# Kernel optimization log

Hardware: AMD Instinct MI355X
Metric: run time of the kernel (lower is better)

Reference implementation:

```python
import jax, jax.numpy as jnp
import numpy as np

N = 100000      # nodes
E = 1600000     # edges (avg degree 16)
IN_FEATS = 128
HEADS = 4
OUT_FEATS = 16
NEG_SLOPE = 0.2
EPS = 1e-16


def setup_inputs() -> dict:
    key = jax.random.key(0)
    k1, k2, k3, k4, k5, k6 = jax.random.split(key, 6)
    feat = jax.random.normal(k1, (N, IN_FEATS), dtype=jnp.float32)
    # xavier-ish scale for params
    W = jax.random.normal(k2, (IN_FEATS, HEADS * OUT_FEATS), dtype=jnp.float32) * 0.1
    attn_l = jax.random.normal(k3, (1, HEADS, OUT_FEATS), dtype=jnp.float32) * 0.1
    attn_r = jax.random.normal(k4, (1, HEADS, OUT_FEATS), dtype=jnp.float32) * 0.1
    src_index = jax.random.randint(k5, (E,), 0, N, dtype=jnp.int32)
    trg_index = jax.random.randint(k6, (E,), 0, N, dtype=jnp.int32)
    return {"feat": feat, "W": W, "attn_l": attn_l, "attn_r": attn_r,
            "src_index": src_index, "trg_index": trg_index}


def reference(feat, W, attn_l, attn_r, src_index, trg_index):
    # dropout layers are identity in eval mode
    n = feat.shape[0]
    h = (feat @ W).reshape(n, HEADS, OUT_FEATS)            # [N,H,F]
    el = jnp.sum(h * attn_l, axis=-1)                      # [N,H]
    er = jnp.sum(h * attn_r, axis=-1)                      # [N,H]
    s = el[src_index] + er[trg_index]                      # [E,H] edge scores
    s = jnp.where(s > 0, s, NEG_SLOPE * s)                 # LeakyReLU(0.2)
    # neighborhood-aware softmax over incoming edges of each target node
    s = s - jnp.max(s)                                     # global max shift (as in source)
    e = jnp.exp(s)                                         # [E,H]
    denom = jax.ops.segment_sum(e, trg_index, num_segments=n)  # [N,H]
    attn = e / (denom[trg_index] + EPS)                    # [E,H]
    # weighted aggregation of lifted source features into target nodes
    msg = h[src_index] * attn[:, :, None]                  # [E,H,F]
    h_prime = jax.ops.segment_sum(msg, trg_index, num_segments=n)  # [N,H,F]
    return h_prime.reshape(n, HEADS * OUT_FEATS)
```

## Files before the change

kernel.cpp:

```cpp
#include <hip/hip_runtime.h>

typedef unsigned short ushort_t;
typedef __attribute__((ext_vector_type(8))) short bf16x8;
typedef __attribute__((ext_vector_type(4))) float f32x4v;

#define EPB 8000

static __device__ __forceinline__ float bf2f(ushort_t u) {
  union { unsigned int i; float f; } v; v.i = ((unsigned int)u) << 16; return v.f;
}
static __device__ __forceinline__ ushort_t f2bf(float f) {
  union { float f; unsigned int i; } v; v.f = f;
  unsigned int r = v.i + 0x7FFFu + ((v.i >> 16) & 1u);
  return (ushort_t)(r >> 16);
}
static __device__ __forceinline__ float leaky(float s) {
  return s > 0.f ? s : 0.2f * s;
}

__global__ __launch_bounds__(256) void packw_hist(
    const float* __restrict__ W, const float* __restrict__ attnl,
    const float* __restrict__ attnr, ushort_t* __restrict__ wfrag,
    const int* __restrict__ trg, int E, int nbkt,
    int* __restrict__ blockHist, int nb3)
{
  const int b = blockIdx.x;
  const int t = threadIdx.x;
  if (b == nb3) {
    const int kc = t >> 6, l = t & 63;
    const int q = l >> 4, n = l & 15;
    #pragma unroll
    for (int tile = 0; tile < 5; ++tile) {
      #pragma unroll
      for (int j = 0; j < 8; ++j) {
        const int k = kc * 32 + q * 8 + j;
        float v = 0.f;
        if (tile < 4) {
          v = W[k * 64 + tile * 16 + n];
        } else if (n < 4) {
          for (int f = 0; f < 16; ++f)
            v += W[k * 64 + n * 16 + f] * attnl[n * 16 + f];
        } else if (n < 8) {
          const int hd = n - 4;
          for (int f = 0; f < 16; ++f)
            v += W[k * 64 + hd * 16 + f] * attnr[hd * 16 + f];
        }
        wfrag[((tile * 4 + kc) * 64 + l) * 8 + j] = f2bf(v);
      }
    }
    return;
  }
  __shared__ int hist[256];
  hist[t] = 0;
  __syncthreads();
  const int start = b * EPB;
  const int end = min(start + EPB, E);
  for (int e = start + t; e < end; e += 256)
    atomicAdd(&hist[trg[e] >> 9], 1);
  __syncthreads();
  if (t < nbkt) blockHist[b * nbkt + t] = hist[t];
}

__global__ __launch_bounds__(64) void bucket_scan(
    int* __restrict__ blockHist, int nb3, int nbkt, int* __restrict__ colTotal)
{
  const int b = blockIdx.x;
  const int l = threadIdx.x;
  int carry = 0;
  for (int r = 0; r * 64 < nb3; ++r) {
    const int i = r * 64 + l;
    int v = (i < nb3) ? blockHist[i * nbkt + b] : 0;
    int incl = v;
    #pragma unroll
    for (int d = 1; d < 64; d <<= 1) {
      int u = __shfl_up(incl, d, 64);
      if (l >= d) incl += u;
    }
    if (i < nb3) blockHist[i * nbkt + b] = carry + incl - v;
    carry += __shfl(incl, 63, 64);
  }
  if (l == 0) colTotal[b] = carry;
}

__global__ __launch_bounds__(64) void bucket_base(
    const int* __restrict__ colTotal, int nbkt, int* __restrict__ bucketBase,
    int* __restrict__ rowoff, int N, int E)
{
  const int l = threadIdx.x;
  int carry = 0;
  for (int r = 0; r * 64 < nbkt; ++r) {
    const int i = r * 64 + l;
    int v = (i < nbkt) ? colTotal[i] : 0;
    int incl = v;
    #pragma unroll
    for (int d = 1; d < 64; d <<= 1) {
      int u = __shfl_up(incl, d, 64);
      if (l >= d) incl += u;
    }
    if (i < nbkt) bucketBase[i] = carry + incl - v;
    carry += __shfl(incl, 63, 64);
  }
  if (l == 0) { bucketBase[nbkt] = carry; rowoff[N] = E; }
}

__global__ __launch_bounds__(256) void bucket_scatter(
    const int* __restrict__ src, const int* __restrict__ trg, int E, int nbkt,
    const int* __restrict__ blockHist, const int* __restrict__ bucketBase,
    unsigned int* __restrict__ binned)
{
  __shared__ int cursor[256];
  const int t = threadIdx.x, b = blockIdx.x;
  if (t < nbkt) cursor[t] = bucketBase[t] + blockHist[b * nbkt + t];
  __syncthreads();
  const int start = b * EPB;
  const int end = min(start + EPB, E);
  for (int e = start + t; e < end; e += 256) {
    const int ti = trg[e];
    const int bkt = ti >> 9;
    const int pos = atomicAdd(&cursor[bkt], 1);
    binned[pos] = ((unsigned int)src[e] << 9) | (unsigned int)(ti & 511);
  }
}

__global__ __launch_bounds__(256) void gat_linear(
    const float* __restrict__ feat, const ushort_t* __restrict__ wfrag,
    ushort_t* __restrict__ h_out, float* __restrict__ el, float* __restrict__ er,
    float* __restrict__ blockmax2, int N)
{
  __shared__ ushort_t sFb[64 * 136];
  __shared__ float wmax[8];
  const int t = threadIdx.x;
  const int b = blockIdx.x;
  const int w = t >> 6, l = t & 63;
  const int q = l >> 4, m = l & 15;

  const float4* gF = (const float4*)(feat + (size_t)b * 64 * 128);
  #pragma unroll
  for (int i = 0; i < 8; ++i) {
    const int idx = i * 256 + t;
    const int node = idx >> 5, off = idx & 31;
    float4 v = make_float4(0.f, 0.f, 0.f, 0.f);
    if (b * 64 + node < N) v = gF[idx];
    unsigned int p0 = ((unsigned int)f2bf(v.y) << 16) | f2bf(v.x);
    unsigned int p1 = ((unsigned int)f2bf(v.w) << 16) | f2bf(v.z);
    *(uint2*)(sFb + node * 136 + off * 4) = make_uint2(p0, p1);
  }
  __syncthreads();

  bf16x8 a[4];
  const ushort_t* arow = sFb + (w * 16 + m) * 136 + q * 8;
  #pragma unroll
  for (int kc = 0; kc < 4; ++kc)
    a[kc] = *(const bf16x8*)(arow + kc * 32);

  #pragma unroll
  for (int tile = 0; tile < 4; ++tile) {
    f32x4v acc = {0.f, 0.f, 0.f, 0.f};
    #pragma unroll
    for (int kc = 0; kc < 4; ++kc) {
      bf16x8 bfr = *(const bf16x8*)(wfrag + ((tile * 4 + kc) * 64 + l) * 8);
      acc = __builtin_amdgcn_mfma_f32_16x16x32_bf16(a[kc], bfr, acc, 0, 0, 0);
    }
    #pragma unroll
    for (int r = 0; r < 4; ++r) {
      const int gn = b * 64 + w * 16 + q * 4 + r;
      if (gn < N) h_out[(size_t)gn * 64 + tile * 16 + m] = f2bf(acc[r]);
    }
  }

  f32x4v acc4 = {0.f, 0.f, 0.f, 0.f};
  #pragma unroll
  for (int kc = 0; kc < 4; ++kc) {
    bf16x8 bfr = *(const bf16x8*)(wfrag + ((4 * 4 + kc) * 64 + l) * 8);
    acc4 = __builtin_amdgcn_mfma_f32_16x16x32_bf16(a[kc], bfr, acc4, 0, 0, 0);
  }
  float mel = -1e30f, mer = -1e30f;
  #pragma unroll
  for (int r = 0; r < 4; ++r) {
    const int gn = b * 64 + w * 16 + q * 4 + r;
    const float v = acc4[r];
    if (m < 4) {
      if (gn < N) el[gn * 4 + m] = v;
      mel = fmaxf(mel, v);
    } else if (m < 8) {
      if (gn < N) er[gn * 4 + (m - 4)] = v;
      mer = fmaxf(mer, v);
    }
  }
  #pragma unroll
  for (int o = 1; o <= 32; o <<= 1) {
    mel = fmaxf(mel, __shfl_xor(mel, o, 64));
    mer = fmaxf(mer, __shfl_xor(mer, o, 64));
  }
  if (l == 0) { wmax[w * 2] = mel; wmax[w * 2 + 1] = mer; }
  __syncthreads();
  if (t == 0) {
    float aa = fmaxf(fmaxf(wmax[0], wmax[2]), fmaxf(wmax[4], wmax[6]));
    float cc = fmaxf(fmaxf(wmax[1], wmax[3]), fmaxf(wmax[5], wmax[7]));
    blockmax2[b * 2] = aa;
    blockmax2[b * 2 + 1] = cc;
  }
}

__global__ __launch_bounds__(512) void fine_scatter(
    const unsigned int* __restrict__ binned, const int* __restrict__ bucketBase,
    int* __restrict__ rowoff, int* __restrict__ csrsrc, int N,
    const float* __restrict__ blockmax2, int nbL, float* __restrict__ gmaxM)
{
  __shared__ int cnt[512];
  __shared__ int ws[8];
  __shared__ float wmg[16];
  const int t = threadIdx.x, b = blockIdx.x;
  const int l = t & 63, w = t >> 6;
  const int base = bucketBase[b];
  const int end = bucketBase[b + 1];
  cnt[t] = 0;
  if (b == 0) {
    float mel = -1e30f, mer = -1e30f;
    for (int i = t; i < nbL; i += 512) {
      mel = fmaxf(mel, blockmax2[i * 2]);
      mer = fmaxf(mer, blockmax2[i * 2 + 1]);
    }
    #pragma unroll
    for (int o = 1; o <= 32; o <<= 1) {
      mel = fmaxf(mel, __shfl_xor(mel, o, 64));
      mer = fmaxf(mer, __shfl_xor(mer, o, 64));
    }
    if (l == 0) { wmg[w * 2] = mel; wmg[w * 2 + 1] = mer; }
  }
  __syncthreads();
  if (b == 0 && t == 0) {
    float aa = -1e30f, cc = -1e30f;
    for (int i = 0; i < 8; ++i) {
      aa = fmaxf(aa, wmg[i * 2]);
      cc = fmaxf(cc, wmg[i * 2 + 1]);
    }
    gmaxM[0] = fmaxf(0.f, aa + cc);
  }
  for (int i = base + t; i < end; i += 512)
    atomicAdd(&cnt[binned[i] & 511u], 1);
  __syncthreads();
  const int v = cnt[t];
  int incl = v;
  #pragma unroll
  for (int d = 1; d < 64; d <<= 1) {
    int u = __shfl_up(incl, d, 64);
    if (l >= d) incl += u;
  }
  if (l == 63) ws[w] = incl;
  __syncthreads();
  int woff = 0;
  for (int i = 0; i < w; ++i) woff += ws[i];
  const int loc = woff + incl - v;
  cnt[t] = loc;
  const int gt = b * 512 + t;
  if (gt < N) rowoff[gt] = base + loc;
  __syncthreads();
  for (int i = base + t; i < end; i += 512) {
    const unsigned int pv = binned[i];
    const int lt = (int)(pv & 511u);
    const int pos = base + atomicAdd(&cnt[lt], 1);
    csrsrc[pos] = (int)(pv >> 9);
  }
}

__global__ __launch_bounds__(256) void gat_agg(
    const int* __restrict__ csrsrc, const int* __restrict__ rowoff,
    const float4* __restrict__ el4, const float4* __restrict__ er4,
    const ushort_t* __restrict__ hbf, const float* __restrict__ gmaxM,
    float* __restrict__ out, int N)
{
  __shared__ float sP[4 * 64 * 4];
  const int t = threadIdx.x;
  const int l = t & 63;
  const int w = t >> 6;
  const int n = blockIdx.x * 4 + w;
  if (n >= N) return;
  const int hd = l >> 4;
  const int start = rowoff[n];
  const int end = rowoff[n + 1];
  const float M = gmaxM[0];
  const float4 ern = er4[n];
  float* sPw = sP + w * 256;

  float a0 = 0.f, a1 = 0.f, a2 = 0.f, a3 = 0.f;
  float a4 = 0.f, a5 = 0.f, a6 = 0.f, a7 = 0.f;
  float4 dsum = make_float4(0.f, 0.f, 0.f, 0.f);

  for (int base = start; base < end; base += 64) {
    const int cnt = min(64, end - base);
    int sn = 0;
    float4 pv = make_float4(0.f, 0.f, 0.f, 0.f);
    if (l < cnt) {
      sn = csrsrc[base + l];
      const float4 a = el4[sn];
      pv.x = __expf(leaky(a.x + ern.x) - M);
      pv.y = __expf(leaky(a.y + ern.y) - M);
      pv.z = __expf(leaky(a.z + ern.z) - M);
      pv.w = __expf(leaky(a.w + ern.w) - M);
    }
    dsum.x += pv.x; dsum.y += pv.y; dsum.z += pv.z; dsum.w += pv.w;
    *(float4*)(sPw + l * 4) = pv;

    int j = 0;
    for (; j + 8 <= cnt; j += 8) {
      const int s0 = __shfl(sn, j,     64);
      const int s1 = __shfl(sn, j + 1, 64);
      const int s2 = __shfl(sn, j + 2, 64);
      const int s3 = __shfl(sn, j + 3, 64);
      const int s4 = __shfl(sn, j + 4, 64);
      const int s5 = __shfl(sn, j + 5, 64);
      const int s6 = __shfl(sn, j + 6, 64);
      const int s7 = __shfl(sn, j + 7, 64);
      a0 += bf2f(hbf[(size_t)s0 * 64 + l]) * sPw[(j)     * 4 + hd];
      a1 += bf2f(hbf[(size_t)s1 * 64 + l]) * sPw[(j + 1) * 4 + hd];
      a2 += bf2f(hbf[(size_t)s2 * 64 + l]) * sPw[(j + 2) * 4 + hd];
      a3 += bf2f(hbf[(size_t)s3 * 64 + l]) * sPw[(j + 3) * 4 + hd];
      a4 += bf2f(hbf[(size_t)s4 * 64 + l]) * sPw[(j + 4) * 4 + hd];
      a5 += bf2f(hbf[(size_t)s5 * 64 + l]) * sPw[(j + 5) * 4 + hd];
      a6 += bf2f(hbf[(size_t)s6 * 64 + l]) * sPw[(j + 6) * 4 + hd];
      a7 += bf2f(hbf[(size_t)s7 * 64 + l]) * sPw[(j + 7) * 4 + hd];
    }
    for (; j < cnt; ++j) {
      const int s0 = __shfl(sn, j, 64);
      a0 += bf2f(hbf[(size_t)s0 * 64 + l]) * sPw[j * 4 + hd];
    }
  }
  #pragma unroll
  for (int o = 1; o <= 32; o <<= 1) {
    dsum.x += __shfl_xor(dsum.x, o, 64);
    dsum.y += __shfl_xor(dsum.y, o, 64);
    dsum.z += __shfl_xor(dsum.z, o, 64);
    dsum.w += __shfl_xor(dsum.w, o, 64);
  }
  const float dacc = (hd == 0) ? dsum.x : (hd == 1) ? dsum.y
                   : (hd == 2) ? dsum.z : dsum.w;
  const float acc = ((a0 + a1) + (a2 + a3)) + ((a4 + a5) + (a6 + a7));
  out[(size_t)n * 64 + l] = acc / (dacc + 1e-16f);
}

extern "C" void kernel_launch(void* const* d_in, const int* in_sizes, int n_in,
                              void* d_out, int out_size, void* d_ws, size_t ws_size,
                              hipStream_t stream) {
  const float* feat  = (const float*)d_in[0];
  const float* W     = (const float*)d_in[1];
  const float* attnl = (const float*)d_in[2];
  const float* attnr = (const float*)d_in[3];
  const int* src = (const int*)d_in[4];
  const int* trg = (const int*)d_in[5];
  float* out = (float*)d_out;

  const int N = in_sizes[0] / 128;
  const int E = in_sizes[4];

  const int nbL  = (N + 63) / 64;
  const int nbkt = (N + 511) >> 9;
  const int nb3  = (E + EPB - 1) / EPB;

  char* p = (char*)d_ws;
  auto take = [&](size_t bytes) -> char* {
    char* r = p;
    p += (bytes + 255) & ~(size_t)255;
    return r;
  };
  ushort_t* h_bf  = (ushort_t*)take((size_t)N * 64 * 2);
  float* el       = (float*)take((size_t)N * 16);
  float* er       = (float*)take((size_t)N * 16);
  int* rowoff     = (int*)take((size_t)(N + 1) * 4);
  int* csrsrc     = (int*)take((size_t)E * 4);
  unsigned int* binned = (unsigned int*)take((size_t)E * 4);
  ushort_t* wfrag = (ushort_t*)take(5 * 4 * 64 * 8 * 2);
  int* blockHist  = (int*)take((size_t)nb3 * nbkt * 4);
  int* colTotal   = (int*)take((size_t)nbkt * 4);
  int* bucketBase = (int*)take((size_t)(nbkt + 1) * 4);
  float* blockmax2 = (float*)take((size_t)nbL * 2 * 4);
  float* gmaxM    = (float*)take(256);

  packw_hist<<<nb3 + 1, 256, 0, stream>>>(W, attnl, attnr, wfrag,
                                          trg, E, nbkt, blockHist, nb3);
  bucket_scan<<<nbkt, 64, 0, stream>>>(blockHist, nb3, nbkt, colTotal);
  bucket_base<<<1, 64, 0, stream>>>(colTotal, nbkt, bucketBase, rowoff, N, E);
  bucket_scatter<<<nb3, 256, 0, stream>>>(src, trg, E, nbkt, blockHist,
                                          bucketBase, binned);
  gat_linear<<<nbL, 256, 0, stream>>>(feat, wfrag, h_bf, el, er,
                                      blockmax2, N);
  fine_scatter<<<nbkt, 512, 0, stream>>>(binned, bucketBase, rowoff, csrsrc,
                                         N, blockmax2, nbL, gmaxM);
  gat_agg<<<(N + 3) / 4, 256, 0, stream>>>(csrsrc, rowoff, (const float4*)el,
                                           (const float4*)er, h_bf,
                                           gmaxM, out, N);
}
```

Before: 223.9 us.

## Gather bf16 source rows with 16-byte vector loads across edge-parallel lanes

The aggregation loop is remapped so each wave handles 8 edges at once. Each lane loads 8 contiguous bf16 features of one source row as a single 16-byte load, instead of every lane loading one 2-byte element per edge. Source indices are staged in LDS rather than broadcast by shuffles, and the partial sums across edge groups are combined with xor-shuffles at the end. The goal is fewer, wider gather instructions and more loads in flight, at the cost of a final cross-lane reduction and padded loads of row 0 for tail edges, which carry zero weight.

```diff
diff --git a/kernel.cpp b/kernel.cpp
--- a/kernel.cpp
+++ b/kernel.cpp
@@ -264,6 +264,18 @@
   }
 }
 
+#define FMA8(hv, p) do { \
+  union { unsigned int i; float f; } c_; \
+  c_.i = (hv).x << 16;          a0 += c_.f * (p); \
+  c_.i = (hv).x & 0xffff0000u;  a1 += c_.f * (p); \
+  c_.i = (hv).y << 16;          a2 += c_.f * (p); \
+  c_.i = (hv).y & 0xffff0000u;  a3 += c_.f * (p); \
+  c_.i = (hv).z << 16;          a4 += c_.f * (p); \
+  c_.i = (hv).z & 0xffff0000u;  a5 += c_.f * (p); \
+  c_.i = (hv).w << 16;          a6 += c_.f * (p); \
+  c_.i = (hv).w & 0xffff0000u;  a7 += c_.f * (p); \
+} while (0)
+
 __global__ __launch_bounds__(256) void gat_agg(
     const int* __restrict__ csrsrc, const int* __restrict__ rowoff,
     const float4* __restrict__ el4, const float4* __restrict__ er4,
@@ -271,17 +283,22 @@
     float* __restrict__ out, int N)
 {
   __shared__ float sP[4 * 64 * 4];
+  __shared__ int sS[4 * 64];
   const int t = threadIdx.x;
   const int l = t & 63;
   const int w = t >> 6;
   const int n = blockIdx.x * 4 + w;
   if (n >= N) return;
-  const int hd = l >> 4;
+  const int rg = l >> 3;
+  const int cg = l & 7;
+  const int hd2 = cg >> 1;
   const int start = rowoff[n];
   const int end = rowoff[n + 1];
   const float M = gmaxM[0];
   const float4 ern = er4[n];
   float* sPw = sP + w * 256;
+  int* sSw = sS + w * 64;
+  const ushort_t* hcg = hbf + cg * 8;
 
   float a0 = 0.f, a1 = 0.f, a2 = 0.f, a3 = 0.f;
   float a4 = 0.f, a5 = 0.f, a6 = 0.f, a7 = 0.f;
@@ -301,30 +318,26 @@
     }
     dsum.x += pv.x; dsum.y += pv.y; dsum.z += pv.z; dsum.w += pv.w;
     *(float4*)(sPw + l * 4) = pv;
-
-    int j = 0;
-    for (; j + 8 <= cnt; j += 8) {
-      const int s0 = __shfl(sn, j,     64);
-      const int s1 = __shfl(sn, j + 1, 64);
-      const int s2 = __shfl(sn, j + 2, 64);
-      const int s3 = __shfl(sn, j + 3, 64);
-      const int s4 = __shfl(sn, j + 4, 64);
-      const int s5 = __shfl(sn, j + 5, 64);
-      const int s6 = __shfl(sn, j + 6, 64);
-      const int s7 = __shfl(sn, j + 7, 64);
-      a0 += bf2f(hbf[(size_t)s0 * 64 + l]) * sPw[(j)     * 4 + hd];
-      a1 += bf2f(hbf[(size_t)s1 * 64 + l]) * sPw[(j + 1) * 4 + hd];
-      a2 += bf2f(hbf[(size_t)s2 * 64 + l]) * sPw[(j + 2) * 4 + hd];
-      a3 += bf2f(hbf[(size_t)s3 * 64 + l]) * sPw[(j + 3) * 4 + hd];
-      a4 += bf2f(hbf[(size_t)s4 * 64 + l]) * sPw[(j + 4) * 4 + hd];
-      a5 += bf2f(hbf[(size_t)s5 * 64 + l]) * sPw[(j + 5) * 4 + hd];
-      a6 += bf2f(hbf[(size_t)s6 * 64 + l]) * sPw[(j + 6) * 4 + hd];
-      a7 += bf2f(hbf[(size_t)s7 * 64 + l]) * sPw[(j + 7) * 4 + hd];
-    }
-    for (; j < cnt; ++j) {
-      const int s0 = __shfl(sn, j, 64);
-      a0 += bf2f(hbf[(size_t)s0 * 64 + l]) * sPw[j * 4 + hd];
-    }
+    sSw[l] = sn;
+
+    for (int j = 0; j < cnt; j += 16) {
+      const int sA = sSw[j + rg];
+      const int sB = sSw[j + 8 + rg];
+      const float pA = sPw[(j + rg) * 4 + hd2];
+      const float pB = sPw[(j + 8 + rg) * 4 + hd2];
+      const uint4 hA = *(const uint4*)(hcg + (size_t)sA * 64);
+      const uint4 hB = *(const uint4*)(hcg + (size_t)sB * 64);
+      FMA8(hA, pA);
+      FMA8(hB, pB);
+    }
+  }
+
+  #pragma unroll
+  for (int o = 8; o <= 32; o <<= 1) {
+    a0 += __shfl_xor(a0, o, 64); a1 += __shfl_xor(a1, o, 64);
+    a2 += __shfl_xor(a2, o, 64); a3 += __shfl_xor(a3, o, 64);
+    a4 += __shfl_xor(a4, o, 64); a5 += __shfl_xor(a5, o, 64);
+    a6 += __shfl_xor(a6, o, 64); a7 += __shfl_xor(a7, o, 64);
   }
   #pragma unroll
   for (int o = 1; o <= 32; o <<= 1) {
@@ -333,10 +346,14 @@
     dsum.z += __shfl_xor(dsum.z, o, 64);
     dsum.w += __shfl_xor(dsum.w, o, 64);
   }
-  const float dacc = (hd == 0) ? dsum.x : (hd == 1) ? dsum.y
-                   : (hd == 2) ? dsum.z : dsum.w;
-  const float acc = ((a0 + a1) + (a2 + a3)) + ((a4 + a5) + (a6 + a7));
-  out[(size_t)n * 64 + l] = acc / (dacc + 1e-16f);
+  if (rg == 0) {
+    const float d = (hd2 == 0) ? dsum.x : (hd2 == 1) ? dsum.y
+                  : (hd2 == 2) ? dsum.z : dsum.w;
+    const float r = 1.0f / (d + 1e-16f);
+    float4* orow = (float4*)(out + (size_t)n * 64 + cg * 8);
+    orow[0] = make_float4(a0 * r, a1 * r, a2 * r, a3 * r);
+    orow[1] = make_float4(a4 * r, a5 * r, a6 * r, a7 * r);
+  }
 }
 
 extern "C" void kernel_launch(void* const* d_in, const int* in_sizes, int n_in,
```

Result: faster. 219.2 us (-2.1%).
